# Kernel optimization log

Hardware: AMD Instinct MI355X
Metric: run time of the kernel (lower is better)

## Reference

```python
import jax, jax.numpy as jnp
import numpy as np

B, T, D = 2, 2048, 2048
H, L = 16, 64
Hd = D // H  # 128
SCALE = 1.0 / np.sqrt(L).astype(np.float32)


def apply_rope(q, k, freqs):
    # q, k: [B, T, H, Hd]; freqs: [T, Hd//2] angles (theta)
    cos = jnp.cos(freqs)[None, :, None, :]  # [1,T,1,Hd/2]
    sin = jnp.sin(freqs)[None, :, None, :]

    def rot(t):
        tr = t.reshape(*t.shape[:-1], Hd // 2, 2)
        a, b = tr[..., 0], tr[..., 1]
        return jnp.stack([a * cos - b * sin, a * sin + b * cos], axis=-1).reshape(t.shape)

    return rot(q), rot(k)


def setup_inputs() -> dict:
    key = jax.random.key(0)
    ks = jax.random.split(key, 16)

    def w(k, shape):
        return jax.random.normal(k, shape, jnp.float32) * 0.02

    x = jax.random.normal(ks[0], (B, T, D), jnp.float32)
    # RoPE angles: theta[t, i] = t / 10000^(2i/Hd)
    inv = 1.0 / (10000.0 ** (jnp.arange(0, Hd, 2, dtype=jnp.float32) / Hd))
    freqs = jnp.arange(T, dtype=jnp.float32)[:, None] * inv[None, :]  # [T, Hd/2]
    # additive causal mask
    mask = jnp.where(jnp.tril(jnp.ones((T, T), bool)), 0.0, -1e9).astype(jnp.float32)

    return dict(
        x=x, freqs=freqs, mask=mask,
        Wq=w(ks[1], (D, D)), bq=jnp.zeros((D,), jnp.float32),
        Wk=w(ks[2], (D, D)), bk=jnp.zeros((D,), jnp.float32),
        Wv=w(ks[3], (D, D)), bv=jnp.zeros((D,), jnp.float32),
        Wo=w(ks[4], (D, D)), bo=jnp.zeros((D,), jnp.float32),
        Wcq=w(ks[5], (Hd, L)), bcq=jnp.zeros((L,), jnp.float32),
        Wck=w(ks[6], (Hd, L)), bck=jnp.zeros((L,), jnp.float32),
        Wcv=w(ks[7], (Hd, L)), bcv=jnp.zeros((L,), jnp.float32),
        Wd=w(ks[8], (L, Hd)), bd=jnp.zeros((Hd,), jnp.float32),
    )


def reference(x, freqs, mask, Wq, bq, Wk, bk, Wv, bv, Wo, bo,
              Wcq, bcq, Wck, bck, Wcv, bcv, Wd, bd):
    b, t, d = x.shape
    q = (x @ Wq + bq).reshape(b, t, H, Hd)
    k = (x @ Wk + bk).reshape(b, t, H, Hd)
    v = (x @ Wv + bv).reshape(b, t, H, Hd)

    q, k = apply_rope(q, k, freqs)

    # per-head latent compression [B,T,H,L]
    q_lat = jnp.einsum('bthd,dl->bthl', q, Wcq) + bcq
    k_lat = jnp.einsum('bthd,dl->bthl', k, Wck) + bck
    v_lat = jnp.einsum('bthd,dl->bthl', v, Wcv) + bcv

    scores = jnp.einsum('bthl,bshl->bhts', q_lat, k_lat) * SCALE
    scores = scores + mask[None, None, :, :]
    attn = jax.nn.softmax(scores, axis=-1)

    out = jnp.einsum('bhts,bshl->bthl', attn, v_lat)  # [B,T,H,L]
    out = jnp.einsum('bthl,lk->bthk', out, Wd) + bd    # decompress -> [B,T,H,Hd]
    out = out.reshape(b, t, d)
    return out @ Wo + bo
```

## Files before the change

kernel.cpp:

```cpp
#include <hip/hip_runtime.h>
#include <hip/hip_bf16.h>

static constexpr int Bsz = 2;
static constexpr int Tn  = 2048;
static constexpr int Dn  = 2048;
static constexpr int Hn  = 16;
static constexpr int Ln  = 64;
static constexpr int Hd  = 128;
static constexpr float SL2E = 0.125f * 1.44269504088896f;

typedef short short8 __attribute__((ext_vector_type(8)));
typedef float f32x4 __attribute__((ext_vector_type(4)));
typedef unsigned short ushort8 __attribute__((ext_vector_type(8)));
typedef unsigned short ushort4v __attribute__((ext_vector_type(4)));
typedef _Float16 half8 __attribute__((ext_vector_type(8)));
typedef unsigned short u16;

__device__ inline unsigned short bf_rne(float f) {
  union { float f; unsigned u; } x; x.f = f;
  unsigned r = x.u + 0x7fffu + ((x.u >> 16) & 1u);
  return (unsigned short)(r >> 16);
}
__device__ inline u16 f16_rne(float f) {
  _Float16 h = (_Float16)f;
  union { _Float16 h; u16 u; } x; x.h = h;
  return x.u;
}
__device__ inline float f16_to_f(u16 u) {
  union { u16 u; _Float16 h; } x; x.u = u;
  return (float)x.h;
}

#define GL(g, l) __builtin_amdgcn_global_load_lds(                     \
    (const __attribute__((address_space(1))) void*)(g),                \
    (__attribute__((address_space(3))) void*)(l), 16, 0, 0)

__global__ void split_h(const float* __restrict__ A, u16* __restrict__ O,
                        int nblk, int Kd) {
  int b = blockIdx.x * 256 + threadIdx.x;
  if (b >= nblk) return;
  int perRow = Kd >> 3;
  int m = b / perRow, gb = b - m * perRow;
  int w = gb >> 2, g = gb & 3;
  const float* src = A + (size_t)m * Kd + (w << 5) + (g << 2);
  float4 v0 = *(const float4*)src;
  float4 v1 = *(const float4*)(src + 16);
  float e[8] = {v0.x, v0.y, v0.z, v0.w, v1.x, v1.y, v1.z, v1.w};
  ushort8 o;
#pragma unroll
  for (int j = 0; j < 8; ++j) o[j] = f16_rne(e[j]);
  *(ushort8*)(O + (size_t)b * 8) = o;
}

__global__ __launch_bounds__(256) void transpose_h(
    const float* __restrict__ W, u16* __restrict__ Th, int Kd, int Nd) {
  __shared__ float t[32][33];
  int k0 = blockIdx.x * 32, n0 = blockIdx.y * 32;
  int i = threadIdx.x;
  {
    int kk = i >> 3, nn = (i & 7) << 2;
    float4 v = *(const float4*)&W[(size_t)(k0 + kk) * Nd + n0 + nn];
    t[kk][nn] = v.x; t[kk][nn + 1] = v.y; t[kk][nn + 2] = v.z; t[kk][nn + 3] = v.w;
  }
  __syncthreads();
  int n = i >> 3, t2 = i & 7;
  int g = t2 >> 1, h = t2 & 1;
  int kbase = h * 16 + g * 4;
  ushort4v o;
#pragma unroll
  for (int j = 0; j < 4; ++j) o[j] = f16_rne(t[kbase + j][n]);
  *(ushort4v*)(Th + (size_t)(n0 + n) * Kd + k0 + t2 * 4) = o;
}

__global__ __launch_bounds__(256) void fold64(
    const float* __restrict__ A, int lda, int a_bx, int a_by,
    const float* __restrict__ B, int ldb, int b_bx, int b_by,
    float* __restrict__ C, int ldc, int c_bx, int c_by) {
  __shared__ float a_lds[64][132];
  __shared__ float b_lds[128][64];
  const int bx = blockIdx.x, by = blockIdx.y, tid = threadIdx.x;
  A += (size_t)bx * a_bx + (size_t)by * a_by;
  B += (size_t)bx * b_bx + (size_t)by * b_by;
  C += (size_t)bx * c_bx + (size_t)by * c_by;
  for (int i = tid; i < 64 * 32; i += 256) {
    int r = i >> 5, c4 = (i & 31) << 2;
    *(float4*)&a_lds[r][c4] = *(const float4*)&A[(size_t)r * lda + c4];
  }
  for (int i = tid; i < 128 * 16; i += 256) {
    int r = i >> 4, c4 = (i & 15) << 2;
    *(float4*)&b_lds[r][c4] = *(const float4*)&B[(size_t)r * ldb + c4];
  }
  __syncthreads();
  const int r = tid >> 2, l0 = (tid & 3) << 4;
  float acc[16] = {};
  for (int k = 0; k < 128; ++k) {
    float av = a_lds[r][k];
    const float* bp = &b_lds[k][l0];
#pragma unroll
    for (int j = 0; j < 16; ++j) acc[j] += av * bp[j];
  }
#pragma unroll
  for (int j4 = 0; j4 < 4; ++j4)
    *(float4*)&C[(size_t)r * ldc + l0 + j4 * 4] = *(float4*)&acc[j4 * 4];
}

__global__ void bias_prep(const float* __restrict__ bv, const float* __restrict__ Wcv,
                          const float* __restrict__ bcv, const float* __restrict__ bd,
                          const float* __restrict__ Wo, const float* __restrict__ bo,
                          float* __restrict__ bias_vf, float* __restrict__ bias_out) {
  int idx = blockIdx.x * 256 + threadIdx.x;
  if (idx < 1024) {
    int h = idx >> 6, l = idx & 63;
    float s = bcv[l];
    for (int j = 0; j < 128; ++j) s += bv[h * 128 + j] * Wcv[j * 64 + l];
    bias_vf[idx] = s;
  } else if (idx < 3072) {
    int n = idx - 1024;
    float s = bo[n];
    for (int k = 0; k < 2048; ++k) s += bd[k & 127] * Wo[(size_t)k * 2048 + n];
    bias_out[n] = s;
  }
}

__global__ __launch_bounds__(256) void gemm_qkv(
    const u16* __restrict__ Af, const u16* __restrict__ Bf,
    u16* __restrict__ cQ, u16* __restrict__ cK, u16* __restrict__ cV,
    const float* __restrict__ bq, const float* __restrict__ bk,
    const float* __restrict__ bvf, int K) {
  __shared__ u16 s[2][2][128 * 32];
  const int tid = threadIdx.x;
  const int lane = tid & 63;
  const int w = tid >> 6, wr = w >> 1, wc = w & 1;
  const int row0 = blockIdx.y * 128, col0 = blockIdx.x * 128;

  const int sr = tid >> 2, sq = tid & 3;
  const int sg = sq ^ ((sr >> 1) & 3);
  const size_t aoff0 = (size_t)(row0 + sr) * K + sg * 8;
  const size_t aoff1 = (size_t)(row0 + sr + 64) * K + sg * 8;
  const size_t boff0 = (size_t)(col0 + sr) * K + sg * 8;
  const size_t boff1 = (size_t)(col0 + sr + 64) * K + sg * 8;
  const int ldst0 = tid * 16, ldst1 = (tid + 256) * 16;

  f32x4 acc[4][4];
#pragma unroll
  for (int i2 = 0; i2 < 4; ++i2)
#pragma unroll
    for (int j2 = 0; j2 < 4; ++j2) acc[i2][j2] = (f32x4){0.f, 0.f, 0.f, 0.f};

  int fa[4], fb[4];
#pragma unroll
  for (int mi = 0; mi < 4; ++mi) {
    int ra = wr * 64 + mi * 16 + (lane & 15);
    fa[mi] = ra * 64 + (((lane >> 4) ^ ((ra >> 1) & 3)) << 4);
    int rb = wc * 64 + mi * 16 + (lane & 15);
    fb[mi] = rb * 64 + (((lane >> 4) ^ ((rb >> 1) & 3)) << 4);
  }

  GL(Af + aoff0, (char*)&s[0][0][0] + ldst0);
  GL(Af + aoff1, (char*)&s[0][0][0] + ldst1);
  GL(Bf + boff0, (char*)&s[0][1][0] + ldst0);
  GL(Bf + boff1, (char*)&s[0][1][0] + ldst1);
  int cur = 0;
  for (int k0 = 0; k0 < K; k0 += 32) {
    __syncthreads();
    if (k0 + 32 < K) {
      const int nb = cur ^ 1;
      GL(Af + aoff0 + k0 + 32, (char*)&s[nb][0][0] + ldst0);
      GL(Af + aoff1 + k0 + 32, (char*)&s[nb][0][0] + ldst1);
      GL(Bf + boff0 + k0 + 32, (char*)&s[nb][1][0] + ldst0);
      GL(Bf + boff1 + k0 + 32, (char*)&s[nb][1][0] + ldst1);
    }
    half8 a[4], b[4];
#pragma unroll
    for (int mi = 0; mi < 4; ++mi) {
      a[mi] = *(const half8*)((const char*)&s[cur][0][0] + fa[mi]);
      b[mi] = *(const half8*)((const char*)&s[cur][1][0] + fb[mi]);
    }
#pragma unroll
    for (int mi = 0; mi < 4; ++mi)
#pragma unroll
      for (int ni = 0; ni < 4; ++ni)
        acc[mi][ni] = __builtin_amdgcn_mfma_f32_16x16x32_f16(a[mi], b[ni], acc[mi][ni], 0, 0, 0);
    cur ^= 1;
  }
  u16* Cp; const float* bp; int ldc, cl0;
  if (col0 < 2048)      { Cp = cQ; bp = bq;  ldc = 2048; cl0 = col0; }
  else if (col0 < 4096) { Cp = cK; bp = bk;  ldc = 2048; cl0 = col0 - 2048; }
  else                  { Cp = cV; bp = bvf; ldc = 1024; cl0 = col0 - 4096; }
#pragma unroll
  for (int ni = 0; ni < 4; ++ni) {
    int c = cl0 + wc * 64 + ni * 16 + (lane & 15);
    float bias = bp[c];
#pragma unroll
    for (int mi = 0; mi < 4; ++mi) {
      int rr = row0 + wr * 64 + mi * 16 + ((lane >> 4) << 2);
#pragma unroll
      for (int r = 0; r < 4; ++r)
        Cp[(size_t)(rr + r) * ldc + c] = f16_rne(acc[mi][ni][r] + bias);
    }
  }
}

__global__ __launch_bounds__(256) void gemm_f16(
    const u16* __restrict__ Af, const u16* __restrict__ Bf,
    const float* __restrict__ bias, float* __restrict__ C,
    int M, int N, int K) {
  __shared__ u16 s[2][2][128 * 32];
  const int tid = threadIdx.x;
  const int lane = tid & 63;
  const int w = tid >> 6, wr = w >> 1, wc = w & 1;
  const int row0 = blockIdx.y * 128, col0 = blockIdx.x * 128;

  const int sr = tid >> 2, sq = tid & 3;
  const int sg = sq ^ ((sr >> 1) & 3);
  const size_t aoff0 = (size_t)(row0 + sr) * K + sg * 8;
  const size_t aoff1 = (size_t)(row0 + sr + 64) * K + sg * 8;
  const size_t boff0 = (size_t)(col0 + sr) * K + sg * 8;
  const size_t boff1 = (size_t)(col0 + sr + 64) * K + sg * 8;
  const int ldst0 = tid * 16, ldst1 = (tid + 256) * 16;

  f32x4 acc[4][4];
#pragma unroll
  for (int i2 = 0; i2 < 4; ++i2)
#pragma unroll
    for (int j2 = 0; j2 < 4; ++j2) acc[i2][j2] = (f32x4){0.f, 0.f, 0.f, 0.f};

  int fa[4], fb[4];
#pragma unroll
  for (int mi = 0; mi < 4; ++mi) {
    int ra = wr * 64 + mi * 16 + (lane & 15);
    fa[mi] = ra * 64 + (((lane >> 4) ^ ((ra >> 1) & 3)) << 4);
    int rb = wc * 64 + mi * 16 + (lane & 15);
    fb[mi] = rb * 64 + (((lane >> 4) ^ ((rb >> 1) & 3)) << 4);
  }

  GL(Af + aoff0, (char*)&s[0][0][0] + ldst0);
  GL(Af + aoff1, (char*)&s[0][0][0] + ldst1);
  GL(Bf + boff0, (char*)&s[0][1][0] + ldst0);
  GL(Bf + boff1, (char*)&s[0][1][0] + ldst1);
  int cur = 0;
  for (int k0 = 0; k0 < K; k0 += 32) {
    __syncthreads();
    if (k0 + 32 < K) {
      const int nb = cur ^ 1;
      GL(Af + aoff0 + k0 + 32, (char*)&s[nb][0][0] + ldst0);
      GL(Af + aoff1 + k0 + 32, (char*)&s[nb][0][0] + ldst1);
      GL(Bf + boff0 + k0 + 32, (char*)&s[nb][1][0] + ldst0);
      GL(Bf + boff1 + k0 + 32, (char*)&s[nb][1][0] + ldst1);
    }
    half8 a[4], b[4];
#pragma unroll
    for (int mi = 0; mi < 4; ++mi) {
      a[mi] = *(const half8*)((const char*)&s[cur][0][0] + fa[mi]);
      b[mi] = *(const half8*)((const char*)&s[cur][1][0] + fb[mi]);
    }
#pragma unroll
    for (int mi = 0; mi < 4; ++mi)
#pragma unroll
      for (int ni = 0; ni < 4; ++ni)
        acc[mi][ni] = __builtin_amdgcn_mfma_f32_16x16x32_f16(a[mi], b[ni], acc[mi][ni], 0, 0, 0);
    cur ^= 1;
  }
#pragma unroll
  for (int ni = 0; ni < 4; ++ni) {
    int c = col0 + wc * 64 + ni * 16 + (lane & 15);
    float bv = bias[c];
#pragma unroll
    for (int mi = 0; mi < 4; ++mi) {
      int rr = row0 + wr * 64 + mi * 16 + ((lane >> 4) << 2);
#pragma unroll
      for (int r = 0; r < 4; ++r)
        C[(size_t)(rr + r) * N + c] = acc[mi][ni][r] + bv;
    }
  }
}

__global__ __launch_bounds__(256) void compress_qk_mfma(
    const u16* __restrict__ src, const u16* __restrict__ WcT,
    const float* __restrict__ bc, const float* __restrict__ freqs,
    u16* __restrict__ dst) {
  __shared__ u16 q_lds[64 * 128];
  __shared__ u16 w_lds[64 * 128];
  const int tid = threadIdx.x;
  const int lane = tid & 63;
  const int w = tid >> 6;
  const int t0 = blockIdx.x * 64;
  const int bh = blockIdx.y, b = bh >> 4, h = bh & 15;

#pragma unroll
  for (int j = 0; j < 4; ++j) {
    int idx = tid + j * 256;
    int row = idx >> 4, slot = idx & 15;
    GL(WcT + (size_t)row * 128 + (size_t)(slot ^ (row & 7)) * 8,
       (char*)w_lds + idx * 16);
  }
  const int r = tid >> 2, seg = tid & 3;
  const u16* qp = src + ((size_t)(b * Tn + t0 + r)) * Dn + h * 128 + seg * 32;
  const float* fp = freqs + (size_t)(t0 + r) * 64 + seg * 16;
  float fr[16];
#pragma unroll
  for (int j = 0; j < 4; ++j) *(float4*)&fr[4 * j] = ((const float4*)fp)[j];
#pragma unroll
  for (int j = 0; j < 8; ++j) {
    ushort4v uv = *(const ushort4v*)(qp + 4 * j);
    float e0 = f16_to_f(uv[0]), e1 = f16_to_f(uv[1]);
    float e2 = f16_to_f(uv[2]), e3 = f16_to_f(uv[3]);
    float s0, c0, s1, c1;
    sincosf(fr[2 * j], &s0, &c0);
    sincosf(fr[2 * j + 1], &s1, &c1);
    ushort4v u;
    u[0] = f16_rne(e0 * c0 - e1 * s0);
    u[1] = f16_rne(e0 * s0 + e1 * c0);
    u[2] = f16_rne(e2 * c1 - e3 * s1);
    u[3] = f16_rne(e2 * s1 + e3 * c1);
    int slot = seg * 4 + (j & 3);
    *(ushort4v*)((char*)q_lds + r * 256 + ((slot ^ (r & 7)) << 4) + (j >> 2) * 8) = u;
  }
  __syncthreads();
  const int l15 = lane & 15, lg = lane >> 4;
  const int arow = w * 16 + l15;
  half8 af[4];
#pragma unroll
  for (int ks = 0; ks < 4; ++ks)
    af[ks] = *(const half8*)((const char*)q_lds + arow * 256 +
                             (((ks * 4 + lg) ^ (arow & 7)) << 4));
  f32x4 acc[4];
#pragma unroll
  for (int ni = 0; ni < 4; ++ni) acc[ni] = (f32x4){0.f, 0.f, 0.f, 0.f};
#pragma unroll
  for (int ni = 0; ni < 4; ++ni) {
    const int brow = ni * 16 + l15;
#pragma unroll
    for (int ks = 0; ks < 4; ++ks) {
      half8 bf = *(const half8*)((const char*)w_lds + brow * 256 +
                                 (((ks * 4 + lg) ^ (brow & 7)) << 4));
      acc[ni] = __builtin_amdgcn_mfma_f32_16x16x32_f16(af[ks], bf, acc[ni], 0, 0, 0);
    }
  }
  __syncthreads();
#pragma unroll
  for (int ni = 0; ni < 4; ++ni) {
    int lat = ni * 16 + l15;
    float bcv = bc[lat];
    int p = (lat & 32) + ((lat >> 2) & 3) * 8 + ((lat >> 4) & 1) * 4 + (lat & 3);
#pragma unroll
    for (int reg = 0; reg < 4; ++reg)
      q_lds[w * 1024 + (lg * 4 + reg) * 64 + p] = f16_rne(acc[ni][reg] + bcv);
  }
  __syncthreads();
#pragma unroll
  for (int j = 0; j < 2; ++j) {
    int idx = tid + j * 256;
    int row = idx >> 3, c8 = idx & 7;
    ushort8 val = *(const ushort8*)&q_lds[row * 64 + c8 * 8];
    *(ushort8*)(dst + ((size_t)bh * Tn + t0 + row) * 64 + c8 * 8) = val;
  }
}

__global__ __launch_bounds__(256) void transpose_v(
    const u16* __restrict__ vlat, u16* __restrict__ vlatT) {
  __shared__ u16 o_lds[64][64];
  const int tid = threadIdx.x;
  const int t0 = blockIdx.x * 64;
  const int bh = blockIdx.y, b = bh >> 4, h = bh & 15;
  const int tt = tid >> 2, lseg = tid & 3;
  const u16* vp = vlat + (size_t)(b * Tn + t0 + tt) * 1024 + h * 64 + lseg * 16;
#pragma unroll
  for (int g = 0; g < 4; ++g) {
    ushort4v u = *(const ushort4v*)(vp + g * 4);
    *(ushort4v*)&o_lds[tt][lseg * 16 + ((g ^ (tt & 3)) << 2)] = u;
  }
  __syncthreads();
  const int lat = tid >> 2, tseg = tid & 3;
  const int tw = tseg >> 1, h4 = tseg & 1;
  u16 vals[16];
#pragma unroll
  for (int i = 0; i < 16; ++i)
    vals[i] = o_lds[tseg * 16 + i][lat ^ ((i & 3) << 2)];
  u16* dp = vlatT + ((size_t)bh * 64 + lat) * Tn + t0 + tw * 32 + h4 * 4;
#pragma unroll
  for (int g = 0; g < 4; ++g) {
    ushort4v u = {vals[g * 4 + 0], vals[g * 4 + 1], vals[g * 4 + 2], vals[g * 4 + 3]};
    *(ushort4v*)(dp + g * 8) = u;
  }
}

__global__ __launch_bounds__(256) void attn_mfma(
    const u16* __restrict__ qlat, const u16* __restrict__ klat,
    const u16* __restrict__ vlatT, float* __restrict__ olatT) {
  __shared__ u16 Ks[64 * 72];
  __shared__ u16 Vs[64 * 72];
  const int tid = threadIdx.x;
  const int lane = tid & 63;
  const int w = tid >> 6;
  const int bh = blockIdx.y;
  const int q0 = (int)(gridDim.x - 1 - blockIdx.x) * 128;
  const int qw = q0 + w * 32;
  const u16* ql = qlat + (size_t)bh * Tn * 64;
  const u16* kl = klat + (size_t)bh * Tn * 64;
  const u16* vt = vlatT + (size_t)bh * 64 * Tn;
  float* ot = olatT + (size_t)bh * 64 * Tn;
  const int l15 = lane & 15, lg = lane >> 4;

  half8 qf[2][2];
#pragma unroll
  for (int nf = 0; nf < 2; ++nf)
#pragma unroll
    for (int ks = 0; ks < 2; ++ks)
      qf[nf][ks] = *(const half8*)(const void*)(ql + (size_t)(qw + nf * 16 + l15) * 64 + (ks * 4 + lg) * 8);

  f32x4 accO[4][2];
#pragma unroll
  for (int mi = 0; mi < 4; ++mi)
#pragma unroll
    for (int nf = 0; nf < 2; ++nf) accO[mi][nf] = (f32x4){0.f, 0.f, 0.f, 0.f};
  float mrow[2] = {-1e30f, -1e30f}, lrow[2] = {0.f, 0.f};

  const int srow = tid >> 2, spair = tid & 3;
  u16* ksw = &Ks[srow * 72 + spair * 16];
  u16* vsw = &Vs[srow * 72 + spair * 16];
  const u16* kgp = kl + (size_t)srow * 64 + spair * 16;
  const u16* vgp = vt + (size_t)srow * Tn + spair * 16;

  ushort8 kr0 = *(const ushort8*)(kgp);
  ushort8 kr1 = *(const ushort8*)(kgp + 8);
  ushort8 vr0 = *(const ushort8*)(vgp);
  ushort8 vr1 = *(const ushort8*)(vgp + 8);

  const int ntiles = q0 / 64 + 2;
  for (int kt = 0; kt < ntiles; ++kt) {
    const int k0 = kt * 64;
    __syncthreads();
    *(ushort8*)ksw       = kr0;
    *(ushort8*)(ksw + 8) = kr1;
    *(ushort8*)vsw       = vr0;
    *(ushort8*)(vsw + 8) = vr1;
    __syncthreads();
    {
      int kn = k0 + 64; kn = kn > (int)Tn - 64 ? (int)Tn - 64 : kn;
      kr0 = *(const ushort8*)(kgp + (size_t)kn * 64);
      kr1 = *(const ushort8*)(kgp + (size_t)kn * 64 + 8);
      vr0 = *(const ushort8*)(vgp + kn);
      vr1 = *(const ushort8*)(vgp + kn + 8);
    }
    if (k0 <= qw + 31) {
      f32x4 s4[4][2];
#pragma unroll
      for (int mi = 0; mi < 4; ++mi) {
        s4[mi][0] = (f32x4){0.f, 0.f, 0.f, 0.f};
        s4[mi][1] = (f32x4){0.f, 0.f, 0.f, 0.f};
      }
      __builtin_amdgcn_s_setprio(1);
#pragma unroll
      for (int ks = 0; ks < 2; ++ks) {
        half8 kf[4];
#pragma unroll
        for (int mi = 0; mi < 4; ++mi)
          kf[mi] = *(const half8*)(const void*)&Ks[(mi * 16 + l15) * 72 + (ks * 4 + lg) * 8];
#pragma unroll
        for (int mi = 0; mi < 4; ++mi) {
          s4[mi][0] = __builtin_amdgcn_mfma_f32_16x16x32_f16(kf[mi], qf[0][ks], s4[mi][0], 0, 0, 0);
          s4[mi][1] = __builtin_amdgcn_mfma_f32_16x16x32_f16(kf[mi], qf[1][ks], s4[mi][1], 0, 0, 0);
        }
      }
      __builtin_amdgcn_s_setprio(0);
      ushort8 pf[2][2];
#pragma unroll
      for (int nf = 0; nf < 2; ++nf) {
        const int qidx = qw + nf * 16 + l15;
        float p[4][4];
        float tmax = -1e30f;
#pragma unroll
        for (int mi = 0; mi < 4; ++mi)
#pragma unroll
          for (int rr = 0; rr < 4; ++rr) {
            int kv = k0 + mi * 16 + lg * 4 + rr;
            float v = s4[mi][nf][rr] * SL2E;
            if (kv > qidx) v = -1e30f;
            p[mi][rr] = v;
            tmax = fmaxf(tmax, v);
          }
        tmax = fmaxf(tmax, __shfl_xor(tmax, 16));
        tmax = fmaxf(tmax, __shfl_xor(tmax, 32));
        float mnew = fmaxf(mrow[nf], tmax);
        float alpha = exp2f(mrow[nf] - mnew);
        mrow[nf] = mnew;
        float psum = 0.f;
        u16 ph[4][4];
#pragma unroll
        for (int mi = 0; mi < 4; ++mi)
#pragma unroll
          for (int rr = 0; rr < 4; ++rr) {
            float e = exp2f(p[mi][rr] - mnew);
            u16 hb = f16_rne(e);
            psum += f16_to_f(hb);
            ph[mi][rr] = hb;
          }
        psum += __shfl_xor(psum, 16);
        psum += __shfl_xor(psum, 32);
        lrow[nf] = lrow[nf] * alpha + psum;
#pragma unroll
        for (int mi = 0; mi < 4; ++mi)
#pragma unroll
          for (int rr = 0; rr < 4; ++rr) accO[mi][nf][rr] *= alpha;
#pragma unroll
        for (int ks = 0; ks < 2; ++ks) {
          ushort8 f;
#pragma unroll
          for (int rr = 0; rr < 4; ++rr) {
            f[rr]     = ph[2 * ks][rr];
            f[4 + rr] = ph[2 * ks + 1][rr];
          }
          pf[nf][ks] = f;
        }
      }
      __builtin_amdgcn_s_setprio(1);
#pragma unroll
      for (int ks = 0; ks < 2; ++ks) {
        half8 vf[4];
#pragma unroll
        for (int mi = 0; mi < 4; ++mi)
          vf[mi] = *(const half8*)(const void*)&Vs[(mi * 16 + l15) * 72 + (ks * 4 + lg) * 8];
#pragma unroll
        for (int mi = 0; mi < 4; ++mi) {
          accO[mi][0] = __builtin_amdgcn_mfma_f32_16x16x32_f16(vf[mi], *(const half8*)&pf[0][ks], accO[mi][0], 0, 0, 0);
          accO[mi][1] = __builtin_amdgcn_mfma_f32_16x16x32_f16(vf[mi], *(const half8*)&pf[1][ks], accO[mi][1], 0, 0, 0);
        }
      }
      __builtin_amdgcn_s_setprio(0);
    }
  }
#pragma unroll
  for (int nf = 0; nf < 2; ++nf) {
    float inv = 1.f / lrow[nf];
    int q = qw + nf * 16 + l15;
#pragma unroll
    for (int mi = 0; mi < 4; ++mi)
#pragma unroll
      for (int rr = 0; rr < 4; ++rr)
        ot[(size_t)(mi * 16 + lg * 4 + rr) * Tn + q] = accO[mi][nf][rr] * inv;
  }
}

__global__ __launch_bounds__(256) void o_split(
    const float* __restrict__ olatT, u16* __restrict__ oh) {
  __shared__ u16 hs[64][64];
  const int tid = threadIdx.x;
  const int q0 = blockIdx.x * 64;
  const int bh = blockIdx.y, b = bh >> 4, h = bh & 15;
  const int lat = tid >> 2, qseg = tid & 3;
  const float* op = olatT + ((size_t)bh * 64 + lat) * Tn + q0 + qseg * 16;
#pragma unroll
  for (int g = 0; g < 4; ++g) {
    float4 v = ((const float4*)op)[g];
    ushort4v u = {f16_rne(v.x), f16_rne(v.y), f16_rne(v.z), f16_rne(v.w)};
    *(ushort4v*)&hs[lat][qseg * 16 + ((g ^ (lat & 3)) << 2)] = u;
  }
  __syncthreads();
  const int qq = tid >> 2, lseg = tid & 3;
  u16 vh[16];
#pragma unroll
  for (int i = 0; i < 16; ++i)
    vh[i] = hs[lseg * 16 + i][qq ^ ((i & 3) << 2)];
  size_t rb = (size_t)(b * Tn + q0 + qq) * 1024 + h * 64 + (lseg >> 1) * 32 + (lseg & 1) * 4;
#pragma unroll
  for (int g = 0; g < 4; ++g) {
    ushort4v u = {vh[g * 4], vh[g * 4 + 1], vh[g * 4 + 2], vh[g * 4 + 3]};
    *(ushort4v*)(oh + rb + g * 8) = u;
  }
}

extern "C" void kernel_launch(void* const* d_in, const int* in_sizes, int n_in,
                              void* d_out, int out_size, void* d_ws, size_t ws_size,
                              hipStream_t stream) {
  const float* x     = (const float*)d_in[0];
  const float* freqs = (const float*)d_in[1];
  const float* Wq  = (const float*)d_in[3];  const float* bq  = (const float*)d_in[4];
  const float* Wk  = (const float*)d_in[5];  const float* bk  = (const float*)d_in[6];
  const float* Wv  = (const float*)d_in[7];  const float* bv  = (const float*)d_in[8];
  const float* Wo  = (const float*)d_in[9];  const float* bo  = (const float*)d_in[10];
  const float* Wcq = (const float*)d_in[11]; const float* bcq = (const float*)d_in[12];
  const float* Wck = (const float*)d_in[13]; const float* bck = (const float*)d_in[14];
  const float* Wcv = (const float*)d_in[15]; const float* bcv = (const float*)d_in[16];
  const float* Wd  = (const float*)d_in[17]; const float* bd  = (const float*)d_in[18];
  float* out = (float*)d_out;

  const size_t BT = (size_t)Bsz * Tn;
  const size_t nQ = BT * Dn;
  const size_t nL = BT * Hn * Ln;
  const size_t nWT = (size_t)5120 * 2048;

  char* ws = (char*)d_ws;
  u16* xf   = (u16*)ws;
  u16* WTf  = xf + nQ;
  float* Wvf = (float*)(WTf + nWT);
  u16* Qh   = (u16*)(Wvf + (size_t)2048 * 1024);
  u16* Kh   = Qh + nQ;
  u16* vlat = Kh + nQ;
  float* bias_vf  = (float*)(vlat + (size_t)4096 * 1024);
  float* bias_out = bias_vf + 1024;
  u16* qlat  = (u16*)(bias_out + 2048);
  u16* klat  = qlat + nL;
  u16* vlatT = klat + nL;
  float* olatT = (float*)(vlatT + nL);
  u16* oh = (u16*)(olatT + nL);
  float* Wdo = (float*)(oh + (size_t)4096 * 1024);
  u16* WdoT = (u16*)(Wdo + (size_t)1024 * 2048);
  u16* WcqT = WdoT + (size_t)2048 * 1024;
  u16* WckT = WcqT + (size_t)64 * 128;

  dim3 blk(256);
  int nblkA = (int)(nQ / 8);

  split_h<<<(nblkA + 255) / 256, blk, 0, stream>>>(x, xf, nblkA, Dn);
  fold64<<<dim3(32, 16), blk, 0, stream>>>(Wv, 2048, 64 * 2048, 128,
                                           Wcv, 64, 0, 0,
                                           Wvf, 1024, 64 * 1024, 64);
  transpose_h<<<dim3(64, 64), blk, 0, stream>>>(Wq, WTf, 2048, 2048);
  transpose_h<<<dim3(64, 64), blk, 0, stream>>>(Wk, WTf + (size_t)2048 * 2048, 2048, 2048);
  transpose_h<<<dim3(64, 32), blk, 0, stream>>>(Wvf, WTf + (size_t)4096 * 2048, 2048, 1024);
  transpose_h<<<dim3(4, 2), blk, 0, stream>>>(Wcq, WcqT, 128, 64);
  transpose_h<<<dim3(4, 2), blk, 0, stream>>>(Wck, WckT, 128, 64);
  bias_prep<<<12, blk, 0, stream>>>(bv, Wcv, bcv, bd, Wo, bo, bias_vf, bias_out);

  gemm_qkv<<<dim3(40, 32), blk, 0, stream>>>(xf, WTf, Qh, Kh, vlat,
                                             bq, bk, bias_vf, 2048);

  dim3 gc(Tn / 64, Bsz * Hn);
  compress_qk_mfma<<<gc, blk, 0, stream>>>(Qh, WcqT, bcq, freqs, qlat);
  compress_qk_mfma<<<gc, blk, 0, stream>>>(Kh, WckT, bck, freqs, klat);
  transpose_v<<<gc, blk, 0, stream>>>(vlat, vlatT);

  attn_mfma<<<dim3(Tn / 128, Bsz * Hn), blk, 0, stream>>>(qlat, klat, vlatT, olatT);

  o_split<<<gc, blk, 0, stream>>>(olatT, oh);
  fold64<<<dim3(32, 16), blk, 0, stream>>>(Wd, 128, 0, 0,
                                           Wo, 2048, 64, 128 * 2048,
                                           Wdo, 2048, 64, 64 * 2048);
  transpose_h<<<dim3(32, 64), blk, 0, stream>>>(Wdo, WdoT, 1024, 2048);
  gemm_f16<<<dim3(16, 32), blk, 0, stream>>>(oh, WdoT, bias_out, out, (int)BT, 2048, 1024);
}
```

Measured before the change: 404.8 us.

## Fuse attention output split into attn kernel and deepen QKV GEMM K-tile

The attention kernel now normalizes its output, converts it to fp16 and writes it straight into the head-interleaved layout used by the output projection, staged through an LDS tile. This removes the separate o_split kernel and the fp32 olatT round trip through global memory. Separately, the QKV GEMM moves from 32 to 64 elements of K per stage with an 8-way XOR swizzle, halving the number of loop iterations and barriers but doubling LDS use per block.

```diff
diff --git a/kernel.cpp b/kernel.cpp
--- a/kernel.cpp
+++ b/kernel.cpp
@@ -16,11 +16,6 @@
 typedef _Float16 half8 __attribute__((ext_vector_type(8)));
 typedef unsigned short u16;
 
-__device__ inline unsigned short bf_rne(float f) {
-  union { float f; unsigned u; } x; x.f = f;
-  unsigned r = x.u + 0x7fffu + ((x.u >> 16) & 1u);
-  return (unsigned short)(r >> 16);
-}
 __device__ inline u16 f16_rne(float f) {
   _Float16 h = (_Float16)f;
   union { _Float16 h; u16 u; } x; x.h = h;
@@ -127,19 +122,21 @@
     u16* __restrict__ cQ, u16* __restrict__ cK, u16* __restrict__ cV,
     const float* __restrict__ bq, const float* __restrict__ bk,
     const float* __restrict__ bvf, int K) {
-  __shared__ u16 s[2][2][128 * 32];
+  __shared__ u16 s[2][2][128 * 64];
   const int tid = threadIdx.x;
   const int lane = tid & 63;
   const int w = tid >> 6, wr = w >> 1, wc = w & 1;
+  const int l15 = lane & 15, lg = lane >> 4;
   const int row0 = blockIdx.y * 128, col0 = blockIdx.x * 128;
 
-  const int sr = tid >> 2, sq = tid & 3;
-  const int sg = sq ^ ((sr >> 1) & 3);
-  const size_t aoff0 = (size_t)(row0 + sr) * K + sg * 8;
-  const size_t aoff1 = (size_t)(row0 + sr + 64) * K + sg * 8;
-  const size_t boff0 = (size_t)(col0 + sr) * K + sg * 8;
-  const size_t boff1 = (size_t)(col0 + sr + 64) * K + sg * 8;
-  const int ldst0 = tid * 16, ldst1 = (tid + 256) * 16;
+  const int sr = tid >> 3, sq = tid & 7;
+  const int sg = sq ^ (sr & 7);
+  size_t aoff[4], boff[4];
+#pragma unroll
+  for (int j = 0; j < 4; ++j) {
+    aoff[j] = (size_t)(row0 + j * 32 + sr) * K + sg * 8;
+    boff[j] = (size_t)(col0 + j * 32 + sr) * K + sg * 8;
+  }
 
   f32x4 acc[4][4];
 #pragma unroll
@@ -147,40 +144,48 @@
 #pragma unroll
     for (int j2 = 0; j2 < 4; ++j2) acc[i2][j2] = (f32x4){0.f, 0.f, 0.f, 0.f};
 
-  int fa[4], fb[4];
+  int fa[4][2], fb[4][2];
 #pragma unroll
   for (int mi = 0; mi < 4; ++mi) {
-    int ra = wr * 64 + mi * 16 + (lane & 15);
-    fa[mi] = ra * 64 + (((lane >> 4) ^ ((ra >> 1) & 3)) << 4);
-    int rb = wc * 64 + mi * 16 + (lane & 15);
-    fb[mi] = rb * 64 + (((lane >> 4) ^ ((rb >> 1) & 3)) << 4);
-  }
-
-  GL(Af + aoff0, (char*)&s[0][0][0] + ldst0);
-  GL(Af + aoff1, (char*)&s[0][0][0] + ldst1);
-  GL(Bf + boff0, (char*)&s[0][1][0] + ldst0);
-  GL(Bf + boff1, (char*)&s[0][1][0] + ldst1);
+    int ra = wr * 64 + mi * 16 + l15;
+    int rb = wc * 64 + mi * 16 + l15;
+#pragma unroll
+    for (int kk = 0; kk < 2; ++kk) {
+      fa[mi][kk] = ra * 128 + (((kk * 4 + lg) ^ (ra & 7)) << 4);
+      fb[mi][kk] = rb * 128 + (((kk * 4 + lg) ^ (rb & 7)) << 4);
+    }
+  }
+
+#pragma unroll
+  for (int j = 0; j < 4; ++j) {
+    GL(Af + aoff[j], (char*)&s[0][0][0] + j * 4096 + tid * 16);
+    GL(Bf + boff[j], (char*)&s[0][1][0] + j * 4096 + tid * 16);
+  }
   int cur = 0;
-  for (int k0 = 0; k0 < K; k0 += 32) {
+  for (int k0 = 0; k0 < K; k0 += 64) {
     __syncthreads();
-    if (k0 + 32 < K) {
+    if (k0 + 64 < K) {
       const int nb = cur ^ 1;
-      GL(Af + aoff0 + k0 + 32, (char*)&s[nb][0][0] + ldst0);
-      GL(Af + aoff1 + k0 + 32, (char*)&s[nb][0][0] + ldst1);
-      GL(Bf + boff0 + k0 + 32, (char*)&s[nb][1][0] + ldst0);
-      GL(Bf + boff1 + k0 + 32, (char*)&s[nb][1][0] + ldst1);
-    }
-    half8 a[4], b[4];
-#pragma unroll
-    for (int mi = 0; mi < 4; ++mi) {
-      a[mi] = *(const half8*)((const char*)&s[cur][0][0] + fa[mi]);
-      b[mi] = *(const half8*)((const char*)&s[cur][1][0] + fb[mi]);
-    }
-#pragma unroll
-    for (int mi = 0; mi < 4; ++mi)
-#pragma unroll
-      for (int ni = 0; ni < 4; ++ni)
-        acc[mi][ni] = __builtin_amdgcn_mfma_f32_16x16x32_f16(a[mi], b[ni], acc[mi][ni], 0, 0, 0);
+#pragma unroll
+      for (int j = 0; j < 4; ++j) {
+        GL(Af + aoff[j] + k0 + 64, (char*)&s[nb][0][0] + j * 4096 + tid * 16);
+        GL(Bf + boff[j] + k0 + 64, (char*)&s[nb][1][0] + j * 4096 + tid * 16);
+      }
+    }
+#pragma unroll
+    for (int kk = 0; kk < 2; ++kk) {
+      half8 a[4], b[4];
+#pragma unroll
+      for (int mi = 0; mi < 4; ++mi) {
+        a[mi] = *(const half8*)((const char*)&s[cur][0][0] + fa[mi][kk]);
+        b[mi] = *(const half8*)((const char*)&s[cur][1][0] + fb[mi][kk]);
+      }
+#pragma unroll
+      for (int mi = 0; mi < 4; ++mi)
+#pragma unroll
+        for (int ni = 0; ni < 4; ++ni)
+          acc[mi][ni] = __builtin_amdgcn_mfma_f32_16x16x32_f16(a[mi], b[ni], acc[mi][ni], 0, 0, 0);
+    }
     cur ^= 1;
   }
   u16* Cp; const float* bp; int ldc, cl0;
@@ -189,11 +194,11 @@
   else                  { Cp = cV; bp = bvf; ldc = 1024; cl0 = col0 - 4096; }
 #pragma unroll
   for (int ni = 0; ni < 4; ++ni) {
-    int c = cl0 + wc * 64 + ni * 16 + (lane & 15);
+    int c = cl0 + wc * 64 + ni * 16 + l15;
     float bias = bp[c];
 #pragma unroll
     for (int mi = 0; mi < 4; ++mi) {
-      int rr = row0 + wr * 64 + mi * 16 + ((lane >> 4) << 2);
+      int rr = row0 + wr * 64 + mi * 16 + lg * 4;
 #pragma unroll
       for (int r = 0; r < 4; ++r)
         Cp[(size_t)(rr + r) * ldc + c] = f16_rne(acc[mi][ni][r] + bias);
@@ -387,19 +392,19 @@
 
 __global__ __launch_bounds__(256) void attn_mfma(
     const u16* __restrict__ qlat, const u16* __restrict__ klat,
-    const u16* __restrict__ vlatT, float* __restrict__ olatT) {
+    const u16* __restrict__ vlatT, u16* __restrict__ oh) {
   __shared__ u16 Ks[64 * 72];
   __shared__ u16 Vs[64 * 72];
+  __shared__ u16 Os[128][72];
   const int tid = threadIdx.x;
   const int lane = tid & 63;
   const int w = tid >> 6;
-  const int bh = blockIdx.y;
+  const int bh = blockIdx.y, b = bh >> 4, h = bh & 15;
   const int q0 = (int)(gridDim.x - 1 - blockIdx.x) * 128;
   const int qw = q0 + w * 32;
   const u16* ql = qlat + (size_t)bh * Tn * 64;
   const u16* kl = klat + (size_t)bh * Tn * 64;
   const u16* vt = vlatT + (size_t)bh * 64 * Tn;
-  float* ot = olatT + (size_t)bh * 64 * Tn;
   const int l15 = lane & 15, lg = lane >> 4;
 
   half8 qf[2][2];
@@ -530,43 +535,28 @@
       __builtin_amdgcn_s_setprio(0);
     }
   }
+  __syncthreads();
 #pragma unroll
   for (int nf = 0; nf < 2; ++nf) {
     float inv = 1.f / lrow[nf];
-    int q = qw + nf * 16 + l15;
-#pragma unroll
-    for (int mi = 0; mi < 4; ++mi)
-#pragma unroll
-      for (int rr = 0; rr < 4; ++rr)
-        ot[(size_t)(mi * 16 + lg * 4 + rr) * Tn + q] = accO[mi][nf][rr] * inv;
-  }
-}
-
-__global__ __launch_bounds__(256) void o_split(
-    const float* __restrict__ olatT, u16* __restrict__ oh) {
-  __shared__ u16 hs[64][64];
-  const int tid = threadIdx.x;
-  const int q0 = blockIdx.x * 64;
-  const int bh = blockIdx.y, b = bh >> 4, h = bh & 15;
-  const int lat = tid >> 2, qseg = tid & 3;
-  const float* op = olatT + ((size_t)bh * 64 + lat) * Tn + q0 + qseg * 16;
-#pragma unroll
-  for (int g = 0; g < 4; ++g) {
-    float4 v = ((const float4*)op)[g];
-    ushort4v u = {f16_rne(v.x), f16_rne(v.y), f16_rne(v.z), f16_rne(v.w)};
-    *(ushort4v*)&hs[lat][qseg * 16 + ((g ^ (lat & 3)) << 2)] = u;
-  }
-  __syncthreads();
-  const int qq = tid >> 2, lseg = tid & 3;
-  u16 vh[16];
-#pragma unroll
-  for (int i = 0; i < 16; ++i)
-    vh[i] = hs[lseg * 16 + i][qq ^ ((i & 3) << 2)];
-  size_t rb = (size_t)(b * Tn + q0 + qq) * 1024 + h * 64 + (lseg >> 1) * 32 + (lseg & 1) * 4;
-#pragma unroll
-  for (int g = 0; g < 4; ++g) {
-    ushort4v u = {vh[g * 4], vh[g * 4 + 1], vh[g * 4 + 2], vh[g * 4 + 3]};
-    *(ushort4v*)(oh + rb + g * 8) = u;
+    int qloc = w * 32 + nf * 16 + l15;
+#pragma unroll
+    for (int mi = 0; mi < 4; ++mi) {
+      int pbase = (mi >> 1) * 32 + lg * 8 + (mi & 1) * 4;
+      ushort4v u;
+#pragma unroll
+      for (int rr = 0; rr < 4; ++rr) u[rr] = f16_rne(accO[mi][nf][rr] * inv);
+      *(ushort4v*)&Os[qloc][pbase] = u;
+    }
+  }
+  __syncthreads();
+  {
+    int rid = tid >> 1, hf = tid & 1;
+    int q = q0 + rid;
+    u16* dstp = oh + ((size_t)(b * Tn + q)) * 1024 + h * 64 + hf * 32;
+#pragma unroll
+    for (int g = 0; g < 4; ++g)
+      *(ushort8*)(dstp + g * 8) = *(const ushort8*)&Os[rid][hf * 32 + g * 8];
   }
 }
 
@@ -602,8 +592,7 @@
   u16* qlat  = (u16*)(bias_out + 2048);
   u16* klat  = qlat + nL;
   u16* vlatT = klat + nL;
-  float* olatT = (float*)(vlatT + nL);
-  u16* oh = (u16*)(olatT + nL);
+  u16* oh = (u16*)(vlatT + nL);
   float* Wdo = (float*)(oh + (size_t)4096 * 1024);
   u16* WdoT = (u16*)(Wdo + (size_t)1024 * 2048);
   u16* WcqT = WdoT + (size_t)2048 * 1024;
@@ -631,9 +620,8 @@
   compress_qk_mfma<<<gc, blk, 0, stream>>>(Kh, WckT, bck, freqs, klat);
   transpose_v<<<gc, blk, 0, stream>>>(vlat, vlatT);
 
-  attn_mfma<<<dim3(Tn / 128, Bsz * Hn), blk, 0, stream>>>(qlat, klat, vlatT, olatT);
-
-  o_split<<<gc, blk, 0, stream>>>(olatT, oh);
+  attn_mfma<<<dim3(Tn / 128, Bsz * Hn), blk, 0, stream>>>(qlat, klat, vlatT, oh);
+
   fold64<<<dim3(32, 16), blk, 0, stream>>>(Wd, 128, 0, 0,
                                            Wo, 2048, 64, 128 * 2048,
                                            Wdo, 2048, 64, 64 * 2048);
```

New measurement: 388.6 us. -4.0%, faster.
